# Performance work log

Hardware: AMD Instinct MI355X
Metric: run time of the kernel (lower is better)

## Reference

```python
import jax, jax.numpy as jnp
import numpy as np

N = 50000      # operations
NI = 20000     # items
NR = 1000      # resources
NM = 500       # materials
OP, IT, RESD, MATD = 128, 128, 64, 32
H, OUT = 256, 128
H2 = H // 2
E_RES, E_MAT, E_PREC = 100000, 100000, 800000


def mlp2(x, W1, b1, W2, b2):
    # Linear -> ReLU -> Linear
    return jax.nn.relu(x @ W1 + b1) @ W2 + b2


def setup_inputs():
    key = jax.random.key(0)
    ks = jax.random.split(key, 40)
    r = lambda i, s: jax.random.normal(ks[i], s, jnp.float32)
    w = lambda i, s: jax.random.normal(ks[i], s, jnp.float32) * 0.02
    inp = {
        "operations": r(0, (N, OP)),
        "items": r(1, (NI, IT)),
        "materials": r(2, (NM, MATD)),
        "resources": r(3, (NR, RESD)),
        "related_items": jax.random.randint(ks[4], (N,), 0, NI),
        "res_op_idx": jax.random.randint(ks[5], (E_RES,), 0, N),
        "res_res_idx": jax.random.randint(ks[6], (E_RES,), 0, NR),
        "mat_op_idx": jax.random.randint(ks[7], (E_MAT,), 0, N),
        "mat_mat_idx": jax.random.randint(ks[8], (E_MAT,), 0, NM),
        "prec_src": jax.random.randint(ks[9], (E_PREC,), 0, N),
        "prec_dst": jax.random.randint(ks[10], (E_PREC,), 0, N),
        "w_self1": w(11, (OP, H)), "b_self1": jnp.zeros((H,), jnp.float32),
        "w_self2": w(12, (H, OUT)), "b_self2": jnp.zeros((OUT,), jnp.float32),
        "w_item1": w(13, (IT, H)), "b_item1": jnp.zeros((H,), jnp.float32),
        "w_item2": w(14, (H, OUT)), "b_item2": jnp.zeros((OUT,), jnp.float32),
        "w_pred1": w(15, (OP, H)), "b_pred1": jnp.zeros((H,), jnp.float32),
        "w_pred2": w(16, (H, OUT)), "b_pred2": jnp.zeros((OUT,), jnp.float32),
        "w_succ1": w(17, (OP, H)), "b_succ1": jnp.zeros((H,), jnp.float32),
        "w_succ2": w(18, (H, OUT)), "b_succ2": jnp.zeros((OUT,), jnp.float32),
        "w_res1": w(19, (RESD, H)), "b_res1": jnp.zeros((H,), jnp.float32),
        "w_res2": w(20, (H, RESD)), "b_res2": jnp.zeros((RESD,), jnp.float32),
        "w_mat1": w(21, (MATD, H)), "b_mat1": jnp.zeros((H,), jnp.float32),
        "w_mat2": w(22, (H, MATD)), "b_mat2": jnp.zeros((MATD,), jnp.float32),
        "w_c1": w(23, (4 * OUT + RESD + MATD, H)), "b_c1": jnp.zeros((H,), jnp.float32),
        "w_c2": w(24, (H, H2)), "b_c2": jnp.zeros((H2,), jnp.float32),
        "w_c3": w(25, (H2, OUT)), "b_c3": jnp.zeros((OUT,), jnp.float32),
    }
    return inp


def reference(operations, items, materials, resources, related_items,
              res_op_idx, res_res_idx, mat_op_idx, mat_mat_idx, prec_src, prec_dst,
              w_self1, b_self1, w_self2, b_self2,
              w_item1, b_item1, w_item2, b_item2,
              w_pred1, b_pred1, w_pred2, b_pred2,
              w_succ1, b_succ1, w_succ2, b_succ2,
              w_res1, b_res1, w_res2, b_res2,
              w_mat1, b_mat1, w_mat2, b_mat2,
              w_c1, b_c1, w_c2, b_c2, w_c3, b_c3):
    n = operations.shape[0]
    self_emb = mlp2(operations, w_self1, b_self1, w_self2, b_self2)           # [N, OUT]
    item_emb = mlp2(items[related_items], w_item1, b_item1, w_item2, b_item2) # [N, OUT]
    # materials -> operations aggregation (scatter-sum over mat edges)
    agg_mat = jax.ops.segment_sum(materials[mat_mat_idx], mat_op_idx, num_segments=n)
    mat_emb = mlp2(agg_mat, w_mat1, b_mat1, w_mat2, b_mat2)                   # [N, MATD]
    # resources -> operations aggregation
    agg_res = jax.ops.segment_sum(resources[res_res_idx], res_op_idx, num_segments=n)
    res_emb = mlp2(agg_res, w_res1, b_res1, w_res2, b_res2)                   # [N, RESD]
    # predecessors: gather operations[edge[1]], scatter onto edge[0]
    agg_pred = jax.ops.segment_sum(operations[prec_dst], prec_src, num_segments=n)
    pred_emb = mlp2(agg_pred, w_pred1, b_pred1, w_pred2, b_pred2)             # [N, OUT]
    # successors: gather operations[edge[0]], scatter onto edge[1]
    agg_succ = jax.ops.segment_sum(operations[prec_src], prec_dst, num_segments=n)
    succ_emb = mlp2(agg_succ, w_succ1, b_succ1, w_succ2, b_succ2)             # [N, OUT]
    x = jnp.concatenate([pred_emb, succ_emb, res_emb, mat_emb, item_emb, self_emb], axis=-1)
    h = jax.nn.relu(x @ w_c1 + b_c1)
    h = jax.nn.relu(h @ w_c2 + b_c2)
    return h @ w_c3 + b_c3
```

## Files before the change

### kernel.cpp

```cpp
#include <hip/hip_runtime.h>
#include <hip/hip_bf16.h>

typedef __attribute__((ext_vector_type(8))) short short8;
typedef __attribute__((ext_vector_type(4))) float f32x4;
using bf16 = __hip_bfloat16;


__device__ __forceinline__ short f2bf(float f) {
  union { float f; unsigned u; } v; v.f = f;
  unsigned r = (v.u + 0x7fffu + ((v.u >> 16) & 1u)) >> 16;
  return (short)r;
}
__device__ __forceinline__ float bf2f(short s) {
  union { unsigned u; float f; } x;
  x.u = ((unsigned)(unsigned short)s) << 16;
  return x.f;
}

struct WDesc { const float* src; int K; int C; int dstoff; };
struct WDescs14 { WDesc w[14]; };

struct PrepArgs {
  const float* ops_src; bf16* ops_dst; int nops4;
  const float* items_src; bf16* items_dst; int nitems4;
  WDescs14 wd; short* wf;
  int* tmp; int ntmp;
};

__global__ __launch_bounds__(256) void prep_kernel(PrepArgs P) {
  const int bx = blockIdx.x;
  switch (blockIdx.y) {
    case 0: {
      int i = bx * 256 + threadIdx.x;
      if (i >= P.nops4) return;
      f32x4 v = *reinterpret_cast<const f32x4*>(P.ops_src + (size_t)i * 4);
      uint2 u;
      u.x = (unsigned)(unsigned short)f2bf(v.x) | ((unsigned)(unsigned short)f2bf(v.y) << 16);
      u.y = (unsigned)(unsigned short)f2bf(v.z) | ((unsigned)(unsigned short)f2bf(v.w) << 16);
      *reinterpret_cast<uint2*>(P.ops_dst + (size_t)i * 4) = u;
    } break;
    case 1: {
      int i = bx * 256 + threadIdx.x;
      if (i >= P.nitems4) return;
      f32x4 v = *reinterpret_cast<const f32x4*>(P.items_src + (size_t)i * 4);
      uint2 u;
      u.x = (unsigned)(unsigned short)f2bf(v.x) | ((unsigned)(unsigned short)f2bf(v.y) << 16);
      u.y = (unsigned)(unsigned short)f2bf(v.z) | ((unsigned)(unsigned short)f2bf(v.w) << 16);
      *reinterpret_cast<uint2*>(P.items_dst + (size_t)i * 4) = u;
    } break;
    case 2: {
      if (bx >= 76 * 14) return;
      WDesc d = P.wd.w[bx / 76];
      int KC = d.K >> 5, CT = d.C >> 4;
      int t = (bx % 76) * 256 + threadIdx.x;
      if (t >= KC * CT * 64) return;
      int lane = t & 63, tile = t >> 6;
      int kc = tile / CT, ct = tile - kc * CT;
      int g = lane >> 4, lp = lane & 15;
      short8 v;
#pragma unroll
      for (int j = 0; j < 8; ++j)
        v[j] = f2bf(d.src[(size_t)(kc * 32 + g * 8 + j) * d.C + ct * 16 + lp]);
      *reinterpret_cast<short8*>(P.wf + d.dstoff + (size_t)t * 8) = v;
    } break;
    default: {
      int i = bx * 256 + threadIdx.x;
      if (i < P.ntmp) P.tmp[i] = 0;
    } break;
  }
}

struct EdgeList { const int* dst; const int* src; int* counts; int* col; int E; };
struct EdgeLists4 { EdgeList l[4]; };

__global__ __launch_bounds__(256) void count4v_kernel(EdgeLists4 ls) {
  EdgeList l = ls.l[blockIdx.y];
  int e0 = (blockIdx.x * 256 + threadIdx.x) * 4;
  if (e0 + 4 <= l.E) {
    int4 d = *reinterpret_cast<const int4*>(l.dst + e0);
    atomicAdd(&l.counts[d.x], 1);
    atomicAdd(&l.counts[d.y], 1);
    atomicAdd(&l.counts[d.z], 1);
    atomicAdd(&l.counts[d.w], 1);
  } else {
    for (int e = e0; e < l.E; ++e) atomicAdd(&l.counts[l.dst[e]], 1);
  }
}

__global__ __launch_bounds__(256) void chunksum_kernel(
    const int* __restrict__ counts, int* __restrict__ bsum, int n, int nchunk) {
  const int t = blockIdx.y;
  const int* cnt = counts + (size_t)t * n;
  int base = blockIdx.x * 1024;
  int s = 0;
  for (int j = threadIdx.x; j < 1024; j += 256) {
    int i = base + j;
    if (i < n) s += cnt[i];
  }
#pragma unroll
  for (int off = 32; off > 0; off >>= 1) s += __shfl_down(s, off, 64);
  __shared__ int ws[4];
  const int lane = threadIdx.x & 63, wid = threadIdx.x >> 6;
  if (lane == 0) ws[wid] = s;
  __syncthreads();
  if (threadIdx.x == 0)
    bsum[(size_t)t * nchunk + blockIdx.x] = ws[0] + ws[1] + ws[2] + ws[3];
}

__global__ __launch_bounds__(1024) void scanfinal2_kernel(
    const int* __restrict__ counts, const int* __restrict__ bsum,
    int* __restrict__ offsets, int* __restrict__ cursor, int n, int nchunk) {
  const int t = blockIdx.y;
  const int* cnt = counts + (size_t)t * n;
  __shared__ int wsum[16];
  __shared__ int base_s;
  const int lane = threadIdx.x & 63, wid = threadIdx.x >> 6;
  if (wid == 0) {
    int b = (lane < blockIdx.x) ? bsum[(size_t)t * nchunk + lane] : 0;
#pragma unroll
    for (int off = 32; off > 0; off >>= 1) b += __shfl_down(b, off, 64);
    if (lane == 0) base_s = b;
  }
  int i = blockIdx.x * 1024 + threadIdx.x;
  int v = (i < n) ? cnt[i] : 0;
  int x = v;
#pragma unroll
  for (int off = 1; off < 64; off <<= 1) {
    int u = __shfl_up(x, off, 64);
    if (lane >= off) x += u;
  }
  if (lane == 63) wsum[wid] = x;
  __syncthreads();
  if (wid == 0 && lane < 16) {
    int w = wsum[lane];
#pragma unroll
    for (int off = 1; off < 16; off <<= 1) {
      int u = __shfl_up(w, off, 16);
      if (lane >= off) w += u;
    }
    wsum[lane] = w;
  }
  __syncthreads();
  int wpre = (wid == 0) ? 0 : wsum[wid - 1];
  int val = base_s + wpre + x - v;
  if (i < n) {
    offsets[(size_t)t * (n + 1) + i] = val;
    cursor[(size_t)t * n + i] = val;
    if (i == n - 1) offsets[(size_t)t * (n + 1) + n] = val + v;
  }
}

__global__ __launch_bounds__(256) void fill4v_kernel(EdgeLists4 ls) {
  EdgeList l = ls.l[blockIdx.y];
  int e0 = (blockIdx.x * 256 + threadIdx.x) * 4;
  if (e0 + 4 <= l.E) {
    int4 d = *reinterpret_cast<const int4*>(l.dst + e0);
    int4 s = *reinterpret_cast<const int4*>(l.src + e0);
    int p0 = atomicAdd(&l.counts[d.x], 1);
    int p1 = atomicAdd(&l.counts[d.y], 1);
    int p2 = atomicAdd(&l.counts[d.z], 1);
    int p3 = atomicAdd(&l.counts[d.w], 1);
    l.col[p0] = s.x;
    l.col[p1] = s.y;
    l.col[p2] = s.z;
    l.col[p3] = s.w;
  } else {
    for (int e = e0; e < l.E; ++e) {
      int p = atomicAdd(&l.counts[l.dst[e]], 1);
      l.col[p] = l.src[e];
    }
  }
}

__device__ __forceinline__ void agg128_dev(
    const bf16* __restrict__ tab, const int* __restrict__ col,
    const int* __restrict__ offs, bf16* __restrict__ out, int n) {
  const int lane = threadIdx.x & 63;
  const int wid = threadIdx.x >> 6;
  const int r = blockIdx.x * 4 + wid;
  if (r >= n) return;
  const int slot = lane >> 4, lp = lane & 15;
  const int beg = offs[r], end = offs[r + 1];
  float acc[8] = {0.f, 0.f, 0.f, 0.f, 0.f, 0.f, 0.f, 0.f};
  float acc2[8] = {0.f, 0.f, 0.f, 0.f, 0.f, 0.f, 0.f, 0.f};
  float acc3[8] = {0.f, 0.f, 0.f, 0.f, 0.f, 0.f, 0.f, 0.f};
  float acc4[8] = {0.f, 0.f, 0.f, 0.f, 0.f, 0.f, 0.f, 0.f};
  int e = beg;
  for (; e + 16 <= end; e += 16) {
    int c0 = col[e + slot];
    int c1 = col[e + 4 + slot];
    int c2 = col[e + 8 + slot];
    int c3 = col[e + 12 + slot];
    short8 v0 = *reinterpret_cast<const short8*>(tab + (size_t)c0 * 128 + lp * 8);
    short8 v1 = *reinterpret_cast<const short8*>(tab + (size_t)c1 * 128 + lp * 8);
    short8 v2 = *reinterpret_cast<const short8*>(tab + (size_t)c2 * 128 + lp * 8);
    short8 v3 = *reinterpret_cast<const short8*>(tab + (size_t)c3 * 128 + lp * 8);
#pragma unroll
    for (int j = 0; j < 8; ++j) {
      acc[j] += bf2f(v0[j]);
      acc2[j] += bf2f(v1[j]);
      acc3[j] += bf2f(v2[j]);
      acc4[j] += bf2f(v3[j]);
    }
  }
  for (; e + 8 <= end; e += 8) {
    int c0 = col[e + slot];
    int c1 = col[e + 4 + slot];
    short8 v0 = *reinterpret_cast<const short8*>(tab + (size_t)c0 * 128 + lp * 8);
    short8 v1 = *reinterpret_cast<const short8*>(tab + (size_t)c1 * 128 + lp * 8);
#pragma unroll
    for (int j = 0; j < 8; ++j) {
      acc[j] += bf2f(v0[j]);
      acc2[j] += bf2f(v1[j]);
    }
  }
  for (; e < end; e += 4) {
    int idx = e + slot;
    if (idx < end) {
      int cc = col[idx];
      short8 v = *reinterpret_cast<const short8*>(tab + (size_t)cc * 128 + lp * 8);
#pragma unroll
      for (int j = 0; j < 8; ++j) acc[j] += bf2f(v[j]);
    }
  }
#pragma unroll
  for (int j = 0; j < 8; ++j) acc[j] = (acc[j] + acc2[j]) + (acc3[j] + acc4[j]);
#pragma unroll
  for (int j = 0; j < 8; ++j) {
    acc[j] += __shfl_xor(acc[j], 16, 64);
    acc[j] += __shfl_xor(acc[j], 32, 64);
  }
  if (slot == 0) {
    short8 sv;
#pragma unroll
    for (int j = 0; j < 8; ++j) sv[j] = f2bf(acc[j]);
    *reinterpret_cast<short8*>(out + (size_t)r * 128 + lp * 8) = sv;
  }
}

template <int D, int LPR>
__device__ __forceinline__ void agg_small_dev(
    const float* __restrict__ tab, const int* __restrict__ col,
    const int* __restrict__ offsets, bf16* __restrict__ out, int n) {
  constexpr int RPB = 256 / LPR;
  const int lane = threadIdx.x % LPR;
  const int r = blockIdx.x * RPB + threadIdx.x / LPR;
  if (r >= n) return;
  const int beg = offsets[r], end = offsets[r + 1];
  float2 acc = make_float2(0.f, 0.f);
  for (int e = beg; e < end; ++e) {
    int s = col[e];
    float2 v = *reinterpret_cast<const float2*>(tab + (size_t)s * D + lane * 2);
    acc.x += v.x;
    acc.y += v.y;
  }
  unsigned u = (unsigned)(unsigned short)f2bf(acc.x) |
               ((unsigned)(unsigned short)f2bf(acc.y) << 16);
  *reinterpret_cast<unsigned*>(out + (size_t)r * D + lane * 2) = u;
}

struct AggArgs {
  const bf16* ops_tab;
  const float* res_tab;
  const float* mat_tab;
  const int *col_pred, *col_succ, *col_res, *col_mat;
  const int *offs_pred, *offs_succ, *offs_res, *offs_mat;
  bf16 *agg_pred, *agg_succ, *agg_res, *agg_mat;
  int n;
};

__global__ __launch_bounds__(256) void agg_all_kernel(AggArgs A) {
  switch (blockIdx.y) {
    case 0: agg128_dev(A.ops_tab, A.col_pred, A.offs_pred, A.agg_pred, A.n); break;
    case 1: agg128_dev(A.ops_tab, A.col_succ, A.offs_succ, A.agg_succ, A.n); break;
    case 2: agg_small_dev<64, 32>(A.res_tab, A.col_res, A.offs_res, A.agg_res, A.n); break;
    default: agg_small_dev<32, 16>(A.mat_tab, A.col_mat, A.offs_mat, A.agg_mat, A.n); break;
  }
}

template <int K, int O, bool GATHER>
__device__ __forceinline__ void mlp2_dev(
    const bf16* __restrict__ X, const int* __restrict__ gidx,
    const short* __restrict__ W1f, const float* __restrict__ B1,
    const short* __restrict__ W2f, const float* __restrict__ B2,
    bf16* __restrict__ xbuf, int ooff, int tile, int lane, char* hw) {
  constexpr int KC = K / 32;
  constexpr int KC2 = 8;
  constexpr int OT = O / 16;
  const int g = lane >> 4, lp = lane & 15;
  const int row0 = tile * 16;

  short8 a[KC];
  {
    int srow = GATHER ? gidx[row0 + lp] : (row0 + lp);
    const bf16* xp = X + (size_t)srow * K + g * 8;
#pragma unroll
    for (int kc = 0; kc < KC; ++kc)
      a[kc] = *reinterpret_cast<const short8*>(xp + kc * 32);
  }

#pragma unroll
  for (int ct = 0; ct < 16; ++ct) {
    float bv = B1[ct * 16 + lp];
    f32x4 acc = {bv, bv, bv, bv};
#pragma unroll
    for (int kc = 0; kc < KC; ++kc) {
      short8 b = *reinterpret_cast<const short8*>(
          W1f + ((size_t)(kc * 16 + ct) * 64 + lane) * 8);
      acc = __builtin_amdgcn_mfma_f32_16x16x32_bf16(a[kc], b, acc, 0, 0, 0);
    }
#pragma unroll
    for (int r = 0; r < 4; ++r) {
      int rr = g * 4 + r;
      int byte = rr * 512 + (ct * 16 + lp) * 2;
      byte ^= (rr & 7) << 4;
      *reinterpret_cast<short*>(hw + byte) = f2bf(fmaxf(acc[r], 0.f));
    }
  }
  asm volatile("s_waitcnt lgkmcnt(0)" ::: "memory");
  __builtin_amdgcn_sched_barrier(0);

  short8 a2[KC2];
#pragma unroll
  for (int kc = 0; kc < KC2; ++kc) {
    int byte = lp * 512 + (kc * 32 + g * 8) * 2;
    byte ^= (lp & 7) << 4;
    a2[kc] = *reinterpret_cast<const short8*>(hw + byte);
  }
#pragma unroll
  for (int ot = 0; ot < OT; ++ot) {
    float bv = B2[ot * 16 + lp];
    f32x4 acc = {bv, bv, bv, bv};
#pragma unroll
    for (int kc = 0; kc < KC2; ++kc) {
      short8 b = *reinterpret_cast<const short8*>(
          W2f + ((size_t)(kc * OT + ot) * 64 + lane) * 8);
      acc = __builtin_amdgcn_mfma_f32_16x16x32_bf16(a2[kc], b, acc, 0, 0, 0);
    }
#pragma unroll
    for (int r = 0; r < 4; ++r) {
      int rr = g * 4 + r;
      *reinterpret_cast<short*>(xbuf + (size_t)(row0 + rr) * 608 + ooff + ot * 16 + lp) =
          f2bf(acc[r]);
    }
  }
}

struct Mlp6Args {
  const bf16 *agg_pred, *agg_succ, *agg_res, *agg_mat, *items_bf, *ops_bf;
  const int* related;
  const short* wf;
  const float *b_pred1, *b_pred2, *b_succ1, *b_succ2, *b_res1, *b_res2;
  const float *b_mat1, *b_mat2, *b_item1, *b_item2, *b_self1, *b_self2;
  bf16* xbuf;
  int ntiles;
};

__global__ __launch_bounds__(256) void mlp6_kernel(Mlp6Args A) {
  __shared__ short hbuf[4 * 16 * 256];
  const int lane = threadIdx.x & 63, wid = threadIdx.x >> 6;
  int tile = blockIdx.x * 4 + wid;
  if (tile >= A.ntiles) tile = A.ntiles - 1;
  char* hw = (char*)(hbuf + wid * (16 * 256));
  const short* wf = A.wf;
  switch (blockIdx.y) {
    case 0: mlp2_dev<128, 128, false>(A.agg_pred, nullptr, wf + 65536, A.b_pred1,
                                      wf + 221184, A.b_pred2, A.xbuf, 0, tile, lane, hw); break;
    case 1: mlp2_dev<128, 128, false>(A.agg_succ, nullptr, wf + 98304, A.b_succ1,
                                      wf + 253952, A.b_succ2, A.xbuf, 128, tile, lane, hw); break;
    case 2: mlp2_dev<64, 64, false>(A.agg_res, nullptr, wf + 131072, A.b_res1,
                                    wf + 286720, A.b_res2, A.xbuf, 256, tile, lane, hw); break;
    case 3: mlp2_dev<32, 32, false>(A.agg_mat, nullptr, wf + 147456, A.b_mat1,
                                    wf + 303104, A.b_mat2, A.xbuf, 320, tile, lane, hw); break;
    case 4: mlp2_dev<128, 128, true>(A.items_bf, A.related, wf + 32768, A.b_item1,
                                     wf + 188416, A.b_item2, A.xbuf, 352, tile, lane, hw); break;
    default: mlp2_dev<128, 128, false>(A.ops_bf, nullptr, wf + 0, A.b_self1,
                                       wf + 155648, A.b_self2, A.xbuf, 480, tile, lane, hw); break;
  }
}

__global__ __launch_bounds__(256, 4) void final_kernel(
    const bf16* __restrict__ xbuf,
    const short* __restrict__ Wc1f, const float* __restrict__ B1,
    const short* __restrict__ Wc2f, const float* __restrict__ B2,
    const float* __restrict__ W3, const float* __restrict__ B3,
    float* __restrict__ out, int ntiles) {
  __shared__ short hbuf[4 * 16 * 256];
  const int lane = threadIdx.x & 63, wid = threadIdx.x >> 6;
  int tile = blockIdx.x * 4 + wid;
  if (tile >= ntiles) tile = ntiles - 1;
  const int g = lane >> 4, lp = lane & 15;
  const int row0 = tile * 16;
  char* hw = (char*)(hbuf + wid * (16 * 256));

  {
    const bf16* xp = xbuf + (size_t)(row0 + lp) * 608 + g * 8;
    short8 a[19];
#pragma unroll
    for (int kc = 0; kc < 19; ++kc)
      a[kc] = *reinterpret_cast<const short8*>(xp + kc * 32);
#pragma unroll
    for (int ct = 0; ct < 16; ++ct) {
      float bv = B1[ct * 16 + lp];
      f32x4 acc = {bv, bv, bv, bv};
#pragma unroll
      for (int kc = 0; kc < 19; ++kc) {
        short8 b = *reinterpret_cast<const short8*>(
            Wc1f + ((size_t)(kc * 16 + ct) * 64 + lane) * 8);
        acc = __builtin_amdgcn_mfma_f32_16x16x32_bf16(a[kc], b, acc, 0, 0, 0);
      }
#pragma unroll
      for (int r = 0; r < 4; ++r) {
        int rr = g * 4 + r;
        int byte = rr * 512 + (ct * 16 + lp) * 2;
        byte ^= (rr & 7) << 4;
        *reinterpret_cast<short*>(hw + byte) = f2bf(fmaxf(acc[r], 0.f));
      }
    }
  }
  asm volatile("s_waitcnt lgkmcnt(0)" ::: "memory");
  __builtin_amdgcn_sched_barrier(0);

  {
    short8 a2[8];
#pragma unroll
    for (int kc = 0; kc < 8; ++kc) {
      int byte = lp * 512 + (kc * 32 + g * 8) * 2;
      byte ^= (lp & 7) << 4;
      a2[kc] = *reinterpret_cast<const short8*>(hw + byte);
    }
    asm volatile("s_waitcnt lgkmcnt(0)" ::: "memory");
    __builtin_amdgcn_sched_barrier(0);
    float* h2 = (float*)hw;
#pragma unroll
    for (int ot = 0; ot < 8; ++ot) {
      float bv = B2[ot * 16 + lp];
      f32x4 acc = {bv, bv, bv, bv};
#pragma unroll
      for (int kc = 0; kc < 8; ++kc) {
        short8 b = *reinterpret_cast<const short8*>(
            Wc2f + ((size_t)(kc * 8 + ot) * 64 + lane) * 8);
        acc = __builtin_amdgcn_mfma_f32_16x16x32_bf16(a2[kc], b, acc, 0, 0, 0);
      }
#pragma unroll
      for (int r = 0; r < 4; ++r)
        h2[(g * 4 + r) * 128 + ot * 16 + lp] = fmaxf(acc[r], 0.f);
    }
  }
  asm volatile("s_waitcnt lgkmcnt(0)" ::: "memory");
  __builtin_amdgcn_sched_barrier(0);

  {
    const float* h2 = (const float*)hw;
    const int half = lane >> 5;
    const int c = (lane & 31) * 4;
    const int rbase = half * 8;
    f32x4 acc3[8];
    f32x4 bv = *reinterpret_cast<const f32x4*>(B3 + c);
#pragma unroll
    for (int rr = 0; rr < 8; ++rr) acc3[rr] = bv;
    for (int k0 = 0; k0 < 128; k0 += 4) {
      f32x4 w0 = *reinterpret_cast<const f32x4*>(W3 + (size_t)(k0 + 0) * 128 + c);
      f32x4 w1 = *reinterpret_cast<const f32x4*>(W3 + (size_t)(k0 + 1) * 128 + c);
      f32x4 w2v = *reinterpret_cast<const f32x4*>(W3 + (size_t)(k0 + 2) * 128 + c);
      f32x4 w3v = *reinterpret_cast<const f32x4*>(W3 + (size_t)(k0 + 3) * 128 + c);
#pragma unroll
      for (int rr = 0; rr < 8; ++rr) {
        f32x4 h = *reinterpret_cast<const f32x4*>(&h2[(rbase + rr) * 128 + k0]);
        acc3[rr] += h.x * w0 + h.y * w1 + h.z * w2v + h.w * w3v;
      }
    }
#pragma unroll
    for (int rr = 0; rr < 8; ++rr)
      *reinterpret_cast<f32x4*>(out + (size_t)(row0 + rbase + rr) * 128 + c) = acc3[rr];
  }
}

extern "C" void kernel_launch(void* const* d_in, const int* in_sizes, int n_in,
                              void* d_out, int out_size, void* d_ws,
                              size_t ws_size, hipStream_t stream) {
  const float* operations = (const float*)d_in[0];
  const float* items      = (const float*)d_in[1];
  const float* materials  = (const float*)d_in[2];
  const float* resources  = (const float*)d_in[3];
  const int* related      = (const int*)d_in[4];
  const int* res_op       = (const int*)d_in[5];
  const int* res_res      = (const int*)d_in[6];
  const int* mat_op       = (const int*)d_in[7];
  const int* mat_mat      = (const int*)d_in[8];
  const int* prec_src     = (const int*)d_in[9];
  const int* prec_dst     = (const int*)d_in[10];
  const float* w_self1 = (const float*)d_in[11];
  const float* b_self1 = (const float*)d_in[12];
  const float* w_self2 = (const float*)d_in[13];
  const float* b_self2 = (const float*)d_in[14];
  const float* w_item1 = (const float*)d_in[15];
  const float* b_item1 = (const float*)d_in[16];
  const float* w_item2 = (const float*)d_in[17];
  const float* b_item2 = (const float*)d_in[18];
  const float* w_pred1 = (const float*)d_in[19];
  const float* b_pred1 = (const float*)d_in[20];
  const float* w_pred2 = (const float*)d_in[21];
  const float* b_pred2 = (const float*)d_in[22];
  const float* w_succ1 = (const float*)d_in[23];
  const float* b_succ1 = (const float*)d_in[24];
  const float* w_succ2 = (const float*)d_in[25];
  const float* b_succ2 = (const float*)d_in[26];
  const float* w_res1  = (const float*)d_in[27];
  const float* b_res1  = (const float*)d_in[28];
  const float* w_res2  = (const float*)d_in[29];
  const float* b_res2  = (const float*)d_in[30];
  const float* w_mat1  = (const float*)d_in[31];
  const float* b_mat1  = (const float*)d_in[32];
  const float* w_mat2  = (const float*)d_in[33];
  const float* b_mat2  = (const float*)d_in[34];
  const float* w_c1    = (const float*)d_in[35];
  const float* b_c1    = (const float*)d_in[36];
  const float* w_c2    = (const float*)d_in[37];
  const float* b_c2    = (const float*)d_in[38];
  const float* w_c3    = (const float*)d_in[39];
  const float* b_c3    = (const float*)d_in[40];

  const int N = in_sizes[0] / 128;
  const int NI = in_sizes[1] / 128;
  const int E_RES = in_sizes[5];
  const int E_MAT = in_sizes[7];
  const int E_PREC = in_sizes[9];

  size_t off = 0;
  auto take = [&](size_t bytes) {
    size_t o = off;
    off += (bytes + 63) & ~(size_t)63;
    return o;
  };
  size_t xbuf_off  = take((size_t)N * 608 * 2);
  size_t aggp_off  = take((size_t)N * 128 * 2);
  size_t aggsu_off = take((size_t)N * 128 * 2);
  size_t aggr_off  = take((size_t)N * 64 * 2);
  size_t aggm_off  = take((size_t)N * 32 * 2);
  size_t wf_off    = take((size_t)499712 * 2);
  size_t opsb_off  = take((size_t)N * 128 * 2);
  size_t itemb_off = take((size_t)NI * 128 * 2);
  size_t offs_off  = take((size_t)4 * (N + 1) * 4);
  size_t tmp_off   = take((size_t)4 * N * 4);
  size_t cols_off  = take(((size_t)2 * E_PREC + E_RES + E_MAT) * 4);
  size_t bsum_off  = take((size_t)4 * 64 * 4);

  char* ws = (char*)d_ws;
  bf16* xbuf = (bf16*)(ws + xbuf_off);
  bf16* agg_pred = (bf16*)(ws + aggp_off);
  bf16* agg_succ = (bf16*)(ws + aggsu_off);
  bf16* agg_res  = (bf16*)(ws + aggr_off);
  bf16* agg_mat  = (bf16*)(ws + aggm_off);
  short* wf = (short*)(ws + wf_off);
  bf16* ops_bf   = (bf16*)(ws + opsb_off);
  bf16* items_bf = (bf16*)(ws + itemb_off);
  int* offs = (int*)(ws + offs_off);
  int* tmp  = (int*)(ws + tmp_off);
  int* cols = (int*)(ws + cols_off);
  int* bsum = (int*)(ws + bsum_off);

  int* offs_pred = offs;
  int* offs_succ = offs + (N + 1);
  int* offs_res  = offs + 2 * (N + 1);
  int* offs_mat  = offs + 3 * (N + 1);
  int* cur_pred = tmp;
  int* cur_succ = tmp + N;
  int* cur_res  = tmp + 2 * N;
  int* cur_mat  = tmp + 3 * N;
  int* col_pred = cols;
  int* col_succ = col_pred + E_PREC;
  int* col_res  = col_succ + E_PREC;
  int* col_mat  = col_res + E_RES;

  dim3 blk(256);

  PrepArgs pp;
  pp.ops_src = operations; pp.ops_dst = ops_bf; pp.nops4 = N * 128 / 4;
  pp.items_src = items; pp.items_dst = items_bf; pp.nitems4 = NI * 128 / 4;
  pp.wd.w[0]  = {w_self1, 128, 256, 0};
  pp.wd.w[1]  = {w_item1, 128, 256, 32768};
  pp.wd.w[2]  = {w_pred1, 128, 256, 65536};
  pp.wd.w[3]  = {w_succ1, 128, 256, 98304};
  pp.wd.w[4]  = {w_res1,   64, 256, 131072};
  pp.wd.w[5]  = {w_mat1,   32, 256, 147456};
  pp.wd.w[6]  = {w_self2, 256, 128, 155648};
  pp.wd.w[7]  = {w_item2, 256, 128, 188416};
  pp.wd.w[8]  = {w_pred2, 256, 128, 221184};
  pp.wd.w[9]  = {w_succ2, 256, 128, 253952};
  pp.wd.w[10] = {w_res2,  256,  64, 286720};
  pp.wd.w[11] = {w_mat2,  256,  32, 303104};
  pp.wd.w[12] = {w_c1,    608, 256, 311296};
  pp.wd.w[13] = {w_c2,    256, 128, 466944};
  pp.wf = wf;
  pp.tmp = tmp; pp.ntmp = 4 * N;
  int prepx = (pp.nops4 + 255) / 256;
  prep_kernel<<<dim3(prepx, 4), blk, 0, stream>>>(pp);

  EdgeLists4 els;
  els.l[0] = {prec_src, prec_dst, cur_pred, col_pred, E_PREC};
  els.l[1] = {prec_dst, prec_src, cur_succ, col_succ, E_PREC};
  els.l[2] = {res_op, res_res, cur_res, col_res, E_RES};
  els.l[3] = {mat_op, mat_mat, cur_mat, col_mat, E_MAT};
  int cgx = (E_PREC / 4 + 255) / 256;
  count4v_kernel<<<dim3(cgx, 4), blk, 0, stream>>>(els);
  int nchunk = (N + 1023) / 1024;
  chunksum_kernel<<<dim3(nchunk, 4), blk, 0, stream>>>(tmp, bsum, N, nchunk);
  scanfinal2_kernel<<<dim3(nchunk, 4), dim3(1024), 0, stream>>>(tmp, bsum, offs, tmp, N, nchunk);
  fill4v_kernel<<<dim3(cgx, 4), blk, 0, stream>>>(els);

  AggArgs aa;
  aa.ops_tab = ops_bf; aa.res_tab = resources; aa.mat_tab = materials;
  aa.col_pred = col_pred; aa.col_succ = col_succ; aa.col_res = col_res; aa.col_mat = col_mat;
  aa.offs_pred = offs_pred; aa.offs_succ = offs_succ; aa.offs_res = offs_res; aa.offs_mat = offs_mat;
  aa.agg_pred = agg_pred; aa.agg_succ = agg_succ; aa.agg_res = agg_res; aa.agg_mat = agg_mat;
  aa.n = N;
  agg_all_kernel<<<dim3((N + 3) / 4, 4), blk, 0, stream>>>(aa);

  int ntiles = N / 16;
  int mgrid = (ntiles + 3) / 4;
  Mlp6Args ma;
  ma.agg_pred = agg_pred; ma.agg_succ = agg_succ; ma.agg_res = agg_res; ma.agg_mat = agg_mat;
  ma.items_bf = items_bf; ma.ops_bf = ops_bf; ma.related = related; ma.wf = wf;
  ma.b_pred1 = b_pred1; ma.b_pred2 = b_pred2; ma.b_succ1 = b_succ1; ma.b_succ2 = b_succ2;
  ma.b_res1 = b_res1; ma.b_res2 = b_res2; ma.b_mat1 = b_mat1; ma.b_mat2 = b_mat2;
  ma.b_item1 = b_item1; ma.b_item2 = b_item2; ma.b_self1 = b_self1; ma.b_self2 = b_self2;
  ma.xbuf = xbuf; ma.ntiles = ntiles;
  mlp6_kernel<<<dim3(mgrid, 6), blk, 0, stream>>>(ma);

  final_kernel<<<mgrid, blk, 0, stream>>>(
      xbuf, wf + 311296, b_c1, wf + 466944, b_c2, w_c3, b_c3, (float*)d_out, ntiles);
}
```

Baseline: 580.7 us.

## Two-pass bucketed CSR fill for precedence edges to localize scatter atomics

```diff
diff --git a/kernel.cpp b/kernel.cpp
--- a/kernel.cpp
+++ b/kernel.cpp
@@ -109,7 +109,8 @@
 
 __global__ __launch_bounds__(1024) void scanfinal2_kernel(
     const int* __restrict__ counts, const int* __restrict__ bsum,
-    int* __restrict__ offsets, int* __restrict__ cursor, int n, int nchunk) {
+    int* __restrict__ offsets, int* __restrict__ cursor,
+    int* __restrict__ bcur, int n, int nchunk) {
   const int t = blockIdx.y;
   const int* cnt = counts + (size_t)t * n;
   __shared__ int wsum[16];
@@ -147,6 +148,66 @@
     offsets[(size_t)t * (n + 1) + i] = val;
     cursor[(size_t)t * n + i] = val;
     if (i == n - 1) offsets[(size_t)t * (n + 1) + n] = val + v;
+    if (t < 2 && (i & 127) == 0) bcur[t * 512 + (i >> 7)] = val;
+  }
+}
+
+struct Part2Args {
+  const int *dst0, *src0, *dst1, *src1;
+  int* bcur;
+  unsigned *scr0, *scr1;
+  int E;
+};
+
+__global__ __launch_bounds__(256) void partition2_kernel(Part2Args P) {
+  const int* dst = blockIdx.y ? P.dst1 : P.dst0;
+  const int* src = blockIdx.y ? P.src1 : P.src0;
+  unsigned* scr = blockIdx.y ? P.scr1 : P.scr0;
+  int* bcur = P.bcur + blockIdx.y * 512;
+  int e0 = (blockIdx.x * 256 + threadIdx.x) * 4;
+  if (e0 + 4 <= P.E) {
+    int4 d = *reinterpret_cast<const int4*>(dst + e0);
+    int4 s = *reinterpret_cast<const int4*>(src + e0);
+    int p0 = atomicAdd(&bcur[d.x >> 7], 1);
+    int p1 = atomicAdd(&bcur[d.y >> 7], 1);
+    int p2 = atomicAdd(&bcur[d.z >> 7], 1);
+    int p3 = atomicAdd(&bcur[d.w >> 7], 1);
+    scr[p0] = ((unsigned)d.x << 16) | (unsigned)s.x;
+    scr[p1] = ((unsigned)d.y << 16) | (unsigned)s.y;
+    scr[p2] = ((unsigned)d.z << 16) | (unsigned)s.z;
+    scr[p3] = ((unsigned)d.w << 16) | (unsigned)s.w;
+  } else {
+    for (int e = e0; e < P.E; ++e) {
+      int dd = dst[e];
+      int p = atomicAdd(&bcur[dd >> 7], 1);
+      scr[p] = ((unsigned)dd << 16) | (unsigned)src[e];
+    }
+  }
+}
+
+struct FillLocalArgs {
+  const unsigned *scr0, *scr1;
+  const int *offs0, *offs1;
+  int *cur0, *cur1;
+  int *col0, *col1;
+  int n;
+};
+
+__global__ __launch_bounds__(256) void filllocal_kernel(FillLocalArgs F) {
+  const unsigned* scr = blockIdx.y ? F.scr1 : F.scr0;
+  const int* offs = blockIdx.y ? F.offs1 : F.offs0;
+  int* cur = blockIdx.y ? F.cur1 : F.cur0;
+  int* col = blockIdx.y ? F.col1 : F.col0;
+  int r0 = blockIdx.x << 7;
+  int r1 = r0 + 128;
+  if (r1 > F.n) r1 = F.n;
+  int beg = offs[r0], end = offs[r1];
+  for (int i = beg + (int)threadIdx.x; i < end; i += 256) {
+    unsigned pk = scr[i];
+    int d = (int)(pk >> 16);
+    int s = (int)(pk & 0xffffu);
+    int p = atomicAdd(&cur[d], 1);
+    col[p] = s;
   }
 }
 
@@ -545,6 +606,8 @@
   size_t tmp_off   = take((size_t)4 * N * 4);
   size_t cols_off  = take(((size_t)2 * E_PREC + E_RES + E_MAT) * 4);
   size_t bsum_off  = take((size_t)4 * 64 * 4);
+  size_t bcur_off  = take((size_t)2 * 512 * 4);
+  size_t scr_off   = take((size_t)2 * E_PREC * 4);
 
   char* ws = (char*)d_ws;
   bf16* xbuf = (bf16*)(ws + xbuf_off);
@@ -559,6 +622,8 @@
   int* tmp  = (int*)(ws + tmp_off);
   int* cols = (int*)(ws + cols_off);
   int* bsum = (int*)(ws + bsum_off);
+  int* bcur = (int*)(ws + bcur_off);
+  unsigned* scr = (unsigned*)(ws + scr_off);
 
   int* offs_pred = offs;
   int* offs_succ = offs + (N + 1);
@@ -572,6 +637,8 @@
   int* col_succ = col_pred + E_PREC;
   int* col_res  = col_succ + E_PREC;
   int* col_mat  = col_res + E_RES;
+  unsigned* scr_pred = scr;
+  unsigned* scr_succ = scr + E_PREC;
 
   dim3 blk(256);
 
@@ -606,8 +673,30 @@
   count4v_kernel<<<dim3(cgx, 4), blk, 0, stream>>>(els);
   int nchunk = (N + 1023) / 1024;
   chunksum_kernel<<<dim3(nchunk, 4), blk, 0, stream>>>(tmp, bsum, N, nchunk);
-  scanfinal2_kernel<<<dim3(nchunk, 4), dim3(1024), 0, stream>>>(tmp, bsum, offs, tmp, N, nchunk);
-  fill4v_kernel<<<dim3(cgx, 4), blk, 0, stream>>>(els);
+  scanfinal2_kernel<<<dim3(nchunk, 4), dim3(1024), 0, stream>>>(
+      tmp, bsum, offs, tmp, bcur, N, nchunk);
+
+  Part2Args pa;
+  pa.dst0 = prec_src; pa.src0 = prec_dst;
+  pa.dst1 = prec_dst; pa.src1 = prec_src;
+  pa.bcur = bcur; pa.scr0 = scr_pred; pa.scr1 = scr_succ; pa.E = E_PREC;
+  partition2_kernel<<<dim3(cgx, 2), blk, 0, stream>>>(pa);
+  int nbuckets = (N + 127) / 128;
+  FillLocalArgs fl;
+  fl.scr0 = scr_pred; fl.scr1 = scr_succ;
+  fl.offs0 = offs_pred; fl.offs1 = offs_succ;
+  fl.cur0 = cur_pred; fl.cur1 = cur_succ;
+  fl.col0 = col_pred; fl.col1 = col_succ;
+  fl.n = N;
+  filllocal_kernel<<<dim3(nbuckets, 2), blk, 0, stream>>>(fl);
+
+  EdgeLists4 els2;
+  els2.l[0] = {res_op, res_res, cur_res, col_res, E_RES};
+  els2.l[1] = {mat_op, mat_mat, cur_mat, col_mat, E_MAT};
+  els2.l[2] = els2.l[0];
+  els2.l[3] = els2.l[1];
+  int cgx2 = (E_RES / 4 + 255) / 256;
+  fill4v_kernel<<<dim3(cgx2, 2), blk, 0, stream>>>(els2);
 
   AggArgs aa;
   aa.ops_tab = ops_bf; aa.res_tab = resources; aa.mat_tab = materials;
```

After: 993.9 us. 1.71x slower.
